# Performance work log

Measured on AMD Instinct MI355X. Metric: run time of the kernel, lower is better.

Reference implementation:

```python
import jax, jax.numpy as jnp
import numpy as np
from jax import lax

B, DIM, H, W = 4, 256, 64, 64
K0, K1 = 5, 7


def conv2d(x, w, b, pad, groups=1, dil=1):
    # x [B,C,H,W], w [O, C//groups, kh, kw]
    y = lax.conv_general_dilated(
        x, w, window_strides=(1, 1), padding=[(pad, pad), (pad, pad)],
        rhs_dilation=(dil, dil), dimension_numbers=("NCHW", "OIHW", "NCHW"),
        feature_group_count=groups)
    return y + b[None, :, None, None]


def bilinear_sample(x, py, px):
    # x [B,C,H,W]; py/px [B,H,W] float sample coords; zero padding outside.
    Bn, C, Hh, Ww = x.shape
    y0 = jnp.floor(py)
    x0 = jnp.floor(px)
    ty = py - y0
    tx = px - x0
    xf = x.reshape(Bn, C, Hh * Ww)

    def corner(yi, xi, wt):
        valid = (yi >= 0) & (yi <= Hh - 1) & (xi >= 0) & (xi <= Ww - 1)
        yc = jnp.clip(yi, 0, Hh - 1).astype(jnp.int32)
        xc = jnp.clip(xi, 0, Ww - 1).astype(jnp.int32)
        idx = (yc * Ww + xc).reshape(Bn, 1, Hh * Ww)
        v = jnp.take_along_axis(xf, idx, axis=2).reshape(Bn, C, Hh, Ww)
        return v * (wt * valid.astype(x.dtype))[:, None, :, :]

    return (corner(y0, x0, (1 - ty) * (1 - tx))
            + corner(y0, x0 + 1, (1 - ty) * tx)
            + corner(y0 + 1, x0, ty * (1 - tx))
            + corner(y0 + 1, x0 + 1, ty * tx))


def deform_dw(x, offsets, w, K, pad, dil):
    # Depthwise torchvision DeformConv2d (groups=C, offset_groups=1, no bias).
    # offsets [B, 2*K*K, H, W] interleaved as (dy, dx) per kernel tap.
    Bn, C, Hh, Ww = x.shape
    K2 = K * K
    off = offsets.reshape(Bn, K2, 2, Hh, Ww)
    dy = jnp.transpose(off[:, :, 0], (1, 0, 2, 3))  # [K2,B,H,W]
    dx = jnp.transpose(off[:, :, 1], (1, 0, 2, 3))
    ki = ((jnp.arange(K2) // K) * dil - pad).astype(x.dtype)  # [K2]
    kj = ((jnp.arange(K2) % K) * dil - pad).astype(x.dtype)
    wk = w.reshape(C, K2).T  # [K2, C]
    gy = jnp.arange(Hh, dtype=x.dtype)[None, :, None]  # [1,H,1]
    gx = jnp.arange(Ww, dtype=x.dtype)[None, None, :]  # [1,1,W]

    def body(acc, tap):
        dyk, dxk, kik, kjk, wkk = tap
        py = gy + kik + dyk  # [B,H,W]
        px = gx + kjk + dxk
        s = bilinear_sample(x, py, px)  # [B,C,H,W]
        return acc + s * wkk[None, :, None, None], None

    acc, _ = lax.scan(body, jnp.zeros_like(x), (dy, dx, ki, kj, wk))
    return acc


def deform_block(x, adj_w, adj_b, off_w, off_b, dw, K, pad, dil):
    xc = conv2d(x, adj_w, adj_b, pad=0)                       # 1x1: C -> 2*K*K
    off = conv2d(xc, off_w, off_b, pad=1, groups=2 * K * K)   # depthwise 3x3
    return deform_dw(x, off, dw, K, pad, dil)


def setup_inputs() -> dict:
    key = jax.random.key(0)
    ks = jax.random.split(key, 12)
    rn = lambda k, s, sc: jax.random.normal(k, s, jnp.float32) * sc
    inp = {"x": rn(ks[0], (B, DIM, H, W), 1.0)}
    # block 0 (5x5, pad 2, dil 1)
    c0 = 2 * K0 * K0
    inp["adj_w0"] = rn(ks[1], (c0, DIM, 1, 1), 0.02)
    inp["adj_b0"] = jnp.zeros((c0,), jnp.float32)
    inp["off_w0"] = rn(ks[2], (c0, 1, 3, 3), 0.02)
    inp["off_b0"] = jnp.zeros((c0,), jnp.float32)
    inp["dw0"] = rn(ks[3], (DIM, 1, K0, K0), 0.05)
    # block 1 (7x7, pad 9, dil 3)
    c1 = 2 * K1 * K1
    inp["adj_w1"] = rn(ks[4], (c1, DIM, 1, 1), 0.02)
    inp["adj_b1"] = jnp.zeros((c1,), jnp.float32)
    inp["off_w1"] = rn(ks[5], (c1, 1, 3, 3), 0.02)
    inp["off_b1"] = jnp.zeros((c1,), jnp.float32)
    inp["dw1"] = rn(ks[6], (DIM, 1, K1, K1), 0.05)
    # final 1x1
    inp["w1"] = rn(ks[7], (DIM, DIM, 1, 1), 0.02)
    inp["b1"] = jnp.zeros((DIM,), jnp.float32)
    return inp


def reference(x, adj_w0, adj_b0, off_w0, off_b0, dw0,
              adj_w1, adj_b1, off_w1, off_b1, dw1, w1, b1):
    attn = deform_block(x, adj_w0, adj_b0, off_w0, off_b0, dw0, K0, 2, 1)
    attn = deform_block(attn, adj_w1, adj_b1, off_w1, off_b1, dw1, K1, 9, 3)
    attn = conv2d(attn, w1, b1, pad=0)
    return x * attn
```

## Files before the change

### kernel.cpp

```cpp
#include <hip/hip_runtime.h>
#include <hip/hip_bf16.h>
#include <hip/hip_fp16.h>

typedef __hip_bfloat16 bf16;
typedef unsigned int   u32;
typedef unsigned short u16;

#define HW 4096
#define NB 4

__device__ __forceinline__ float blo(u32 v){ return __uint_as_float(v << 16); }
__device__ __forceinline__ float bhi(u32 v){ return __uint_as_float(v & 0xffff0000u); }
__device__ __forceinline__ u32 pack2(float a, float b){
  union { bf16 h; u16 u; } ua, ub;
  ua.h = __float2bfloat16(a); ub.h = __float2bfloat16(b);
  return (u32)ua.u | ((u32)ub.u << 16);
}

__global__ __launch_bounds__(128) void k_dwT(const float* __restrict__ dw, u32* __restrict__ dwTb, int K2){
  int tt = blockIdx.x;
  int c0 = threadIdx.x * 2;
  dwTb[tt*128 + threadIdx.x] = pack2(dw[(size_t)c0*K2 + tt], dw[(size_t)(c0+1)*K2 + tt]);
}

__global__ __launch_bounds__(256) void k_transpose(const float* __restrict__ x, bf16* __restrict__ xh){
  __shared__ float tile[64][65];
  int t = threadIdx.x, blk = blockIdx.x;
  int ct = blk & 3, pt = (blk >> 2) & 63, b = blk >> 8;
  int lp = t & 63, l4 = t >> 6;
  #pragma unroll
  for (int i = 0; i < 16; ++i){
    int cl = l4 + 4*i;
    tile[cl][lp] = x[((size_t)(b*256 + ct*64 + cl))*HW + pt*64 + lp];
  }
  __syncthreads();
  #pragma unroll
  for (int i = 0; i < 16; ++i){
    int pl = l4 + 4*i;
    xh[((size_t)b*HW + pt*64 + pl)*256 + ct*64 + lp] = __float2bfloat16(tile[lp][pl]);
  }
}

__global__ __launch_bounds__(256) void k_c1x1_nhwc(const bf16* __restrict__ a, const float* __restrict__ w,
                                                   const float* __restrict__ bias, float* __restrict__ out,
                                                   int OC, int OCB){
  __shared__ u32   a2[32*129];
  __shared__ float w2[50*65];
  int t = threadIdx.x;
  int pix0 = blockIdx.x * 32;
  int oc0  = blockIdx.y * OCB;
  int ocnt = min(OCB, OC - oc0);
  const u32* a32 = (const u32*)a;
  int j = t & 127, half = t >> 7;
  #pragma unroll
  for (int ii = 0; ii < 16; ++ii){
    int i = half*16 + ii;
    a2[i*129 + j] = a32[(size_t)(pix0 + i)*128 + j];
  }
  int oc_l = t >> 2, pg = t & 3;
  float acc[8];
  float bv = (oc_l < ocnt) ? bias[oc0 + oc_l] : 0.f;
  #pragma unroll
  for (int q = 0; q < 8; ++q) acc[q] = bv;
  for (int c0 = 0; c0 < 256; c0 += 64){
    __syncthreads();
    for (int idx = t; idx < ocnt*64; idx += 256){
      int o = idx >> 6, jj = idx & 63;
      w2[o*65 + jj] = w[(size_t)(oc0 + o)*256 + c0 + jj];
    }
    __syncthreads();
    if (oc_l < ocnt){
      #pragma unroll 8
      for (int jj2 = 0; jj2 < 32; ++jj2){
        float wlo = w2[oc_l*65 + 2*jj2], whi = w2[oc_l*65 + 2*jj2 + 1];
        #pragma unroll
        for (int q = 0; q < 8; ++q){
          u32 av = a2[(pg*8 + q)*129 + (c0 >> 1) + jj2];
          acc[q] += blo(av)*wlo + bhi(av)*whi;
        }
      }
    }
  }
  if (oc_l < ocnt){
    int b = pix0 >> 12, pr = (pix0 & 4095) + pg*8;
    float* po = out + (size_t)(b*OC + oc0 + oc_l)*HW + pr;
    ((float4*)po)[0] = make_float4(acc[0], acc[1], acc[2], acc[3]);
    ((float4*)po)[1] = make_float4(acc[4], acc[5], acc[6], acc[7]);
  }
}

__global__ __launch_bounds__(256) void k_dw3(const float* __restrict__ in, const float* __restrict__ w,
                                             const float* __restrict__ bias, float* __restrict__ out, int OC){
  int bo = blockIdx.x;
  int oc = bo % OC;
  int p  = blockIdx.y*256 + threadIdx.x;
  int y = p >> 6, x = p & 63;
  const float* ib = in + (size_t)bo*HW;
  float acc = bias[oc];
  #pragma unroll
  for (int dy = 0; dy < 3; ++dy){
    int yy = y + dy - 1;
    if (yy < 0 || yy > 63) continue;
    #pragma unroll
    for (int dx = 0; dx < 3; ++dx){
      int xx = x + dx - 1;
      if (xx < 0 || xx > 63) continue;
      acc += ib[yy*64 + xx] * w[oc*9 + dy*3 + dx];
    }
  }
  out[(size_t)bo*HW + p] = acc;
}

template<int K, int PAD, int DIL, int UNR>
__global__ __launch_bounds__(256) void k_deform_f(
    const bf16* __restrict__ xh, const float* __restrict__ off,
    const u32* __restrict__ dwTb, bf16* __restrict__ oh){
  constexpr int K2 = K*K;
  __shared__ uint2 lw[K2][8];
  __shared__ u16   la[K2][8];
  int t  = threadIdx.x;
  int cg = t & 31;
  int pl = t >> 5;
  int blk = blockIdx.x;
  int b   = blk >> 9;
  int p0  = (blk & 511) * 8;
  for (int e = t; e < 8*K2; e += 256){
    int tt = e >> 3, pxl = e & 7;
    int p  = p0 + pxl;
    int yi = p >> 6, xi = p & 63;
    const float* ob = off + ((size_t)(b*2*K2) + 2*tt)*HW + p;
    float dy = ob[0];
    float dx = ob[HW];
    float py = (float)(yi + (tt/K)*DIL - PAD) + dy;
    float px = (float)(xi + (tt%K)*DIL - PAD) + dx;
    float fy = floorf(py), fx = floorf(px);
    float ty = py - fy, tx = px - fx;
    int iy = (int)fy, ix = (int)fx;
    int sy = min(max(iy, 0), 62);
    int sx = min(max(ix, 0), 62);
    float wy0 = (sy   == iy) ? (1.f-ty) : ((sy   == iy+1) ? ty : 0.f);
    float wy1 = (sy+1 == iy) ? (1.f-ty) : ((sy+1 == iy+1) ? ty : 0.f);
    float wx0 = (sx   == ix) ? (1.f-tx) : ((sx   == ix+1) ? tx : 0.f);
    float wx1 = (sx+1 == ix) ? (1.f-tx) : ((sx+1 == ix+1) ? tx : 0.f);
    u32 lo = (u32)__half_as_ushort(__float2half(wy0*wx0))
           | ((u32)__half_as_ushort(__float2half(wy0*wx1)) << 16);
    u32 hi = (u32)__half_as_ushort(__float2half(wy1*wx0))
           | ((u32)__half_as_ushort(__float2half(wy1*wx1)) << 16);
    lw[tt][pxl] = make_uint2(lo, hi);
    la[tt][pxl] = (u16)(sy*64 + sx);
  }
  __syncthreads();
  const bf16* xb = xh + (size_t)b*HW*256;
  float acc[8];
  #pragma unroll
  for (int j = 0; j < 8; ++j) acc[j] = 0.f;
  for (int t0 = 0; t0 < K2; t0 += UNR){
    #pragma unroll
    for (int u = 0; u < UNR; ++u){
      int tt = t0 + u;
      uint2 wv = lw[tt][pl];
      int   a  = la[tt][pl];
      uint4 dpk = *(const uint4*)&dwTb[tt*128 + cg*4];
      float W00 = __half2float(__ushort_as_half((u16)(wv.x & 0xffffu)));
      float W01 = __half2float(__ushort_as_half((u16)(wv.x >> 16)));
      float W10 = __half2float(__ushort_as_half((u16)(wv.y & 0xffffu)));
      float W11 = __half2float(__ushort_as_half((u16)(wv.y >> 16)));
      const bf16* base = xb + (size_t)a*256 + cg*8;
      uint4 r00 = *(const uint4*)(base);
      uint4 r01 = *(const uint4*)(base + 256);
      uint4 r10 = *(const uint4*)(base + 64*256);
      uint4 r11 = *(const uint4*)(base + 65*256);
      const u32 q00[4] = {r00.x, r00.y, r00.z, r00.w};
      const u32 q01[4] = {r01.x, r01.y, r01.z, r01.w};
      const u32 q10[4] = {r10.x, r10.y, r10.z, r10.w};
      const u32 q11[4] = {r11.x, r11.y, r11.z, r11.w};
      const u32 dq[4]  = {dpk.x, dpk.y, dpk.z, dpk.w};
      #pragma unroll
      for (int q = 0; q < 4; ++q){
        float sl = W00*blo(q00[q]) + W01*blo(q01[q]) + W10*blo(q10[q]) + W11*blo(q11[q]);
        float sh = W00*bhi(q00[q]) + W01*bhi(q01[q]) + W10*bhi(q10[q]) + W11*bhi(q11[q]);
        acc[2*q]   += blo(dq[q]) * sl;
        acc[2*q+1] += bhi(dq[q]) * sh;
      }
    }
  }
  size_t op = ((size_t)b*HW + p0 + pl)*256 + cg*8;
  uint4 ov;
  ov.x = pack2(acc[0], acc[1]); ov.y = pack2(acc[2], acc[3]);
  ov.z = pack2(acc[4], acc[5]); ov.w = pack2(acc[6], acc[7]);
  *(uint4*)(oh + op) = ov;
}

__global__ __launch_bounds__(256) void k_final(const bf16* __restrict__ attnh, const float* __restrict__ w1,
                                               const float* __restrict__ b1, const float* __restrict__ x,
                                               float* __restrict__ out){
  __shared__ float at[256][33];
  __shared__ float wt[256][17];
  int t   = threadIdx.x;
  int blk = blockIdx.x;
  int b   = blk >> 7;
  int p0  = (blk & 127) * 32;
  for (int i = 0; i < 32; ++i)
    at[t][i] = __bfloat162float(attnh[((size_t)b*HW + p0 + i)*256 + t]);
  float acc[32];
  float bv = b1[t];
  for (int i = 0; i < 32; ++i) acc[i] = bv;
  for (int c0 = 0; c0 < 256; c0 += 16){
    __syncthreads();
    for (int k = 0; k < 16; ++k){
      int idx = k*256 + t;
      wt[idx >> 4][idx & 15] = w1[(idx >> 4)*256 + c0 + (idx & 15)];
    }
    __syncthreads();
    for (int j = 0; j < 16; ++j){
      float wv = wt[t][j];
      const float* ar = &at[c0 + j][0];
      for (int i = 0; i < 32; ++i)
        acc[i] += wv * ar[i];
    }
  }
  size_t gi = ((size_t)(b*256 + t))*HW + p0;
  for (int i = 0; i < 32; ++i)
    out[gi + i] = acc[i] * x[gi + i];
}

extern "C" void kernel_launch(void* const* d_in, const int* in_sizes, int n_in,
                              void* d_out, int out_size, void* d_ws, size_t ws_size,
                              hipStream_t stream){
  const float* x   = (const float*)d_in[0];
  const float* aw0 = (const float*)d_in[1];
  const float* ab0 = (const float*)d_in[2];
  const float* ow0 = (const float*)d_in[3];
  const float* ob0 = (const float*)d_in[4];
  const float* dw0 = (const float*)d_in[5];
  const float* aw1 = (const float*)d_in[6];
  const float* ab1 = (const float*)d_in[7];
  const float* ow1 = (const float*)d_in[8];
  const float* ob1 = (const float*)d_in[9];
  const float* dw1 = (const float*)d_in[10];
  const float* w1  = (const float*)d_in[11];
  const float* b1  = (const float*)d_in[12];
  float* O = (float*)d_out;

  const size_t MB8 = 8388608;
  char* ws = (char*)d_ws;
  bf16*  xh    = (bf16*) (ws);
  float* XC1   = (float*)(ws);
  bf16*  A1h   = (bf16*) (ws);
  float* XC0   = (float*)(ws + MB8);
  float* OF0   = (float*)(ws + MB8 + 3276800);
  float* OF1   = (float*)(ws + MB8);
  bf16*  A0h   = (bf16*) (ws + 2*MB8);
  u32*   dwTb0 = (u32*)  (ws + 3*MB8);
  u32*   dwTb1 = (u32*)  (ws + 3*MB8 + 131072);

  k_dwT<<<25, 128, 0, stream>>>(dw0, dwTb0, 25);
  k_dwT<<<49, 128, 0, stream>>>(dw1, dwTb1, 49);
  k_transpose<<<1024, 256, 0, stream>>>(x, xh);
  k_c1x1_nhwc<<<dim3(512, 1), 256, 0, stream>>>(xh, aw0, ab0, XC0, 50, 50);
  k_dw3<<<dim3(NB*50, 16), 256, 0, stream>>>(XC0, ow0, ob0, OF0, 50);
  k_deform_f<5,2,1,5><<<NB*512, 256, 0, stream>>>(xh, OF0, dwTb0, A0h);
  k_c1x1_nhwc<<<dim3(512, 2), 256, 0, stream>>>(A0h, aw1, ab1, XC1, 98, 49);
  k_dw3<<<dim3(NB*98, 16), 256, 0, stream>>>(XC1, ow1, ob1, OF1, 98);
  k_deform_f<7,9,3,7><<<NB*512, 256, 0, stream>>>(A0h, OF1, dwTb1, A1h);
  k_final<<<NB*128, 256, 0, stream>>>(A1h, w1, b1, x, O);
}
```

Before: 322.1 us.

## Fuse second deformable conv with final 1x1 conv and gating multiply

Merges the second depthwise deformable convolution into the final 1x1 pointwise convolution and the x-multiply. Each block keeps its 8-pixel by 256-channel deform result in shared memory and runs the 256x256 matmul from there, so the bf16 intermediate is never written to or read back from global memory. A shared arena is reused for the tap tables and the weight tiles. It also removes the manual tap-loop unroll parameter. The trade-off is that w1 is now reloaded per 8 pixels instead of per 32, which multiplies weight traffic and adds syncs, and the x reads and output writes become narrower 32-byte strided chunks.

```diff
diff --git a/kernel.cpp b/kernel.cpp
--- a/kernel.cpp
+++ b/kernel.cpp
@@ -111,7 +111,7 @@
   out[(size_t)bo*HW + p] = acc;
 }
 
-template<int K, int PAD, int DIL, int UNR>
+template<int K, int PAD, int DIL>
 __global__ __launch_bounds__(256) void k_deform_f(
     const bf16* __restrict__ xh, const float* __restrict__ off,
     const u32* __restrict__ dwTb, bf16* __restrict__ oh){
@@ -154,34 +154,30 @@
   float acc[8];
   #pragma unroll
   for (int j = 0; j < 8; ++j) acc[j] = 0.f;
-  for (int t0 = 0; t0 < K2; t0 += UNR){
+  for (int tt = 0; tt < K2; ++tt){
+    uint2 wv = lw[tt][pl];
+    int   a  = la[tt][pl];
+    uint4 dpk = *(const uint4*)&dwTb[tt*128 + cg*4];
+    float W00 = __half2float(__ushort_as_half((u16)(wv.x & 0xffffu)));
+    float W01 = __half2float(__ushort_as_half((u16)(wv.x >> 16)));
+    float W10 = __half2float(__ushort_as_half((u16)(wv.y & 0xffffu)));
+    float W11 = __half2float(__ushort_as_half((u16)(wv.y >> 16)));
+    const bf16* base = xb + (size_t)a*256 + cg*8;
+    uint4 r00 = *(const uint4*)(base);
+    uint4 r01 = *(const uint4*)(base + 256);
+    uint4 r10 = *(const uint4*)(base + 64*256);
+    uint4 r11 = *(const uint4*)(base + 65*256);
+    const u32 q00[4] = {r00.x, r00.y, r00.z, r00.w};
+    const u32 q01[4] = {r01.x, r01.y, r01.z, r01.w};
+    const u32 q10[4] = {r10.x, r10.y, r10.z, r10.w};
+    const u32 q11[4] = {r11.x, r11.y, r11.z, r11.w};
+    const u32 dq[4]  = {dpk.x, dpk.y, dpk.z, dpk.w};
     #pragma unroll
-    for (int u = 0; u < UNR; ++u){
-      int tt = t0 + u;
-      uint2 wv = lw[tt][pl];
-      int   a  = la[tt][pl];
-      uint4 dpk = *(const uint4*)&dwTb[tt*128 + cg*4];
-      float W00 = __half2float(__ushort_as_half((u16)(wv.x & 0xffffu)));
-      float W01 = __half2float(__ushort_as_half((u16)(wv.x >> 16)));
-      float W10 = __half2float(__ushort_as_half((u16)(wv.y & 0xffffu)));
-      float W11 = __half2float(__ushort_as_half((u16)(wv.y >> 16)));
-      const bf16* base = xb + (size_t)a*256 + cg*8;
-      uint4 r00 = *(const uint4*)(base);
-      uint4 r01 = *(const uint4*)(base + 256);
-      uint4 r10 = *(const uint4*)(base + 64*256);
-      uint4 r11 = *(const uint4*)(base + 65*256);
-      const u32 q00[4] = {r00.x, r00.y, r00.z, r00.w};
-      const u32 q01[4] = {r01.x, r01.y, r01.z, r01.w};
-      const u32 q10[4] = {r10.x, r10.y, r10.z, r10.w};
-      const u32 q11[4] = {r11.x, r11.y, r11.z, r11.w};
-      const u32 dq[4]  = {dpk.x, dpk.y, dpk.z, dpk.w};
-      #pragma unroll
-      for (int q = 0; q < 4; ++q){
-        float sl = W00*blo(q00[q]) + W01*blo(q01[q]) + W10*blo(q10[q]) + W11*blo(q11[q]);
-        float sh = W00*bhi(q00[q]) + W01*bhi(q01[q]) + W10*bhi(q10[q]) + W11*bhi(q11[q]);
-        acc[2*q]   += blo(dq[q]) * sl;
-        acc[2*q+1] += bhi(dq[q]) * sh;
-      }
+    for (int q = 0; q < 4; ++q){
+      float sl = W00*blo(q00[q]) + W01*blo(q01[q]) + W10*blo(q10[q]) + W11*blo(q11[q]);
+      float sh = W00*bhi(q00[q]) + W01*bhi(q01[q]) + W10*bhi(q10[q]) + W11*bhi(q11[q]);
+      acc[2*q]   += blo(dq[q]) * sl;
+      acc[2*q+1] += bhi(dq[q]) * sh;
     }
   }
   size_t op = ((size_t)b*HW + p0 + pl)*256 + cg*8;
@@ -191,37 +187,107 @@
   *(uint4*)(oh + op) = ov;
 }
 
-__global__ __launch_bounds__(256) void k_final(const bf16* __restrict__ attnh, const float* __restrict__ w1,
-                                               const float* __restrict__ b1, const float* __restrict__ x,
-                                               float* __restrict__ out){
-  __shared__ float at[256][33];
-  __shared__ float wt[256][17];
-  int t   = threadIdx.x;
+template<int K, int PAD, int DIL>
+__global__ __launch_bounds__(256) void k_deform_final(
+    const bf16* __restrict__ xh, const float* __restrict__ off,
+    const u32* __restrict__ dwTb, const float* __restrict__ w1,
+    const float* __restrict__ b1, const float* __restrict__ x,
+    float* __restrict__ out){
+  constexpr int K2 = K*K;
+  __shared__ float at[8][260];
+  __shared__ __align__(16) char arena[17408];
+  uint2* lw = (uint2*)arena;
+  u16*   la = (u16*)(arena + (size_t)K2*8*8);
+  float* wt = (float*)arena;
+  int t  = threadIdx.x;
+  int cg = t & 31;
+  int pl = t >> 5;
   int blk = blockIdx.x;
-  int b   = blk >> 7;
-  int p0  = (blk & 127) * 32;
-  for (int i = 0; i < 32; ++i)
-    at[t][i] = __bfloat162float(attnh[((size_t)b*HW + p0 + i)*256 + t]);
-  float acc[32];
+  int b   = blk >> 9;
+  int p0  = (blk & 511) * 8;
+  for (int e = t; e < 8*K2; e += 256){
+    int tt = e >> 3, pxl = e & 7;
+    int p  = p0 + pxl;
+    int yi = p >> 6, xi = p & 63;
+    const float* ob = off + ((size_t)(b*2*K2) + 2*tt)*HW + p;
+    float dy = ob[0];
+    float dx = ob[HW];
+    float py = (float)(yi + (tt/K)*DIL - PAD) + dy;
+    float px = (float)(xi + (tt%K)*DIL - PAD) + dx;
+    float fy = floorf(py), fx = floorf(px);
+    float ty = py - fy, tx = px - fx;
+    int iy = (int)fy, ix = (int)fx;
+    int sy = min(max(iy, 0), 62);
+    int sx = min(max(ix, 0), 62);
+    float wy0 = (sy   == iy) ? (1.f-ty) : ((sy   == iy+1) ? ty : 0.f);
+    float wy1 = (sy+1 == iy) ? (1.f-ty) : ((sy+1 == iy+1) ? ty : 0.f);
+    float wx0 = (sx   == ix) ? (1.f-tx) : ((sx   == ix+1) ? tx : 0.f);
+    float wx1 = (sx+1 == ix) ? (1.f-tx) : ((sx+1 == ix+1) ? tx : 0.f);
+    u32 lo = (u32)__half_as_ushort(__float2half(wy0*wx0))
+           | ((u32)__half_as_ushort(__float2half(wy0*wx1)) << 16);
+    u32 hi = (u32)__half_as_ushort(__float2half(wy1*wx0))
+           | ((u32)__half_as_ushort(__float2half(wy1*wx1)) << 16);
+    lw[tt*8 + pxl] = make_uint2(lo, hi);
+    la[tt*8 + pxl] = (u16)(sy*64 + sx);
+  }
+  __syncthreads();
+  const bf16* xb = xh + (size_t)b*HW*256;
+  float acc[8];
+  #pragma unroll
+  for (int j = 0; j < 8; ++j) acc[j] = 0.f;
+  for (int tt = 0; tt < K2; ++tt){
+    uint2 wv = lw[tt*8 + pl];
+    int   a  = la[tt*8 + pl];
+    uint4 dpk = *(const uint4*)&dwTb[tt*128 + cg*4];
+    float W00 = __half2float(__ushort_as_half((u16)(wv.x & 0xffffu)));
+    float W01 = __half2float(__ushort_as_half((u16)(wv.x >> 16)));
+    float W10 = __half2float(__ushort_as_half((u16)(wv.y & 0xffffu)));
+    float W11 = __half2float(__ushort_as_half((u16)(wv.y >> 16)));
+    const bf16* base = xb + (size_t)a*256 + cg*8;
+    uint4 r00 = *(const uint4*)(base);
+    uint4 r01 = *(const uint4*)(base + 256);
+    uint4 r10 = *(const uint4*)(base + 64*256);
+    uint4 r11 = *(const uint4*)(base + 65*256);
+    const u32 q00[4] = {r00.x, r00.y, r00.z, r00.w};
+    const u32 q01[4] = {r01.x, r01.y, r01.z, r01.w};
+    const u32 q10[4] = {r10.x, r10.y, r10.z, r10.w};
+    const u32 q11[4] = {r11.x, r11.y, r11.z, r11.w};
+    const u32 dq[4]  = {dpk.x, dpk.y, dpk.z, dpk.w};
+    #pragma unroll
+    for (int q = 0; q < 4; ++q){
+      float sl = W00*blo(q00[q]) + W01*blo(q01[q]) + W10*blo(q10[q]) + W11*blo(q11[q]);
+      float sh = W00*bhi(q00[q]) + W01*bhi(q01[q]) + W10*bhi(q10[q]) + W11*bhi(q11[q]);
+      acc[2*q]   += blo(dq[q]) * sl;
+      acc[2*q+1] += bhi(dq[q]) * sh;
+    }
+  }
+  ((float4*)&at[pl][cg*8])[0] = make_float4(acc[0], acc[1], acc[2], acc[3]);
+  ((float4*)&at[pl][cg*8])[1] = make_float4(acc[4], acc[5], acc[6], acc[7]);
+  float acc2[8];
   float bv = b1[t];
-  for (int i = 0; i < 32; ++i) acc[i] = bv;
+  #pragma unroll
+  for (int i = 0; i < 8; ++i) acc2[i] = bv;
   for (int c0 = 0; c0 < 256; c0 += 16){
     __syncthreads();
+    #pragma unroll
     for (int k = 0; k < 16; ++k){
       int idx = k*256 + t;
-      wt[idx >> 4][idx & 15] = w1[(idx >> 4)*256 + c0 + (idx & 15)];
+      wt[(idx >> 4)*17 + (idx & 15)] = w1[(size_t)(idx >> 4)*256 + c0 + (idx & 15)];
     }
     __syncthreads();
+    #pragma unroll 4
     for (int j = 0; j < 16; ++j){
-      float wv = wt[t][j];
-      const float* ar = &at[c0 + j][0];
-      for (int i = 0; i < 32; ++i)
-        acc[i] += wv * ar[i];
+      float wv = wt[t*17 + j];
+      #pragma unroll
+      for (int i = 0; i < 8; ++i)
+        acc2[i] += wv * at[i][c0 + j];
     }
   }
   size_t gi = ((size_t)(b*256 + t))*HW + p0;
-  for (int i = 0; i < 32; ++i)
-    out[gi + i] = acc[i] * x[gi + i];
+  float4 xa = ((const float4*)(x + gi))[0];
+  float4 xb4 = ((const float4*)(x + gi))[1];
+  ((float4*)(out + gi))[0] = make_float4(acc2[0]*xa.x, acc2[1]*xa.y, acc2[2]*xa.z, acc2[3]*xa.w);
+  ((float4*)(out + gi))[1] = make_float4(acc2[4]*xb4.x, acc2[5]*xb4.y, acc2[6]*xb4.z, acc2[7]*xb4.w);
 }
 
 extern "C" void kernel_launch(void* const* d_in, const int* in_sizes, int n_in,
@@ -246,7 +312,6 @@
   char* ws = (char*)d_ws;
   bf16*  xh    = (bf16*) (ws);
   float* XC1   = (float*)(ws);
-  bf16*  A1h   = (bf16*) (ws);
   float* XC0   = (float*)(ws + MB8);
   float* OF0   = (float*)(ws + MB8 + 3276800);
   float* OF1   = (float*)(ws + MB8);
@@ -259,9 +324,8 @@
   k_transpose<<<1024, 256, 0, stream>>>(x, xh);
   k_c1x1_nhwc<<<dim3(512, 1), 256, 0, stream>>>(xh, aw0, ab0, XC0, 50, 50);
   k_dw3<<<dim3(NB*50, 16), 256, 0, stream>>>(XC0, ow0, ob0, OF0, 50);
-  k_deform_f<5,2,1,5><<<NB*512, 256, 0, stream>>>(xh, OF0, dwTb0, A0h);
+  k_deform_f<5,2,1><<<NB*512, 256, 0, stream>>>(xh, OF0, dwTb0, A0h);
   k_c1x1_nhwc<<<dim3(512, 2), 256, 0, stream>>>(A0h, aw1, ab1, XC1, 98, 49);
   k_dw3<<<dim3(NB*98, 16), 256, 0, stream>>>(XC1, ow1, ob1, OF1, 98);
-  k_deform_f<7,9,3,7><<<NB*512, 256, 0, stream>>>(A0h, OF1, dwTb1, A1h);
-  k_final<<<NB*128, 256, 0, stream>>>(A1h, w1, b1, x, O);
-}
+  k_deform_final<7,9,3><<<NB*512, 256, 0, stream>>>(A0h, OF1, dwTb1, w1, b1, x, O);
+}
```

Result: faster. 267.5 us (-17.0%).
